# Performance work log

Measured on AMD Instinct MI355X. Metric: run time of the kernel, lower is better.

## Reference

```python
import jax, jax.numpy as jnp
import numpy as np

# Production-scale dims (see shape_source)
N = 100_000      # total nodes (tokens)
E = 1_600_000    # edges
B = 2_000        # graphs / documents
VOCAB = 50_000
NW = 256         # word_vec width == GraphConv out channels (args.nw)
ENC = 512        # args.enc_nh
K = 100          # args.num_topic
EPS = 1e-5       # BatchNorm eps


def setup_inputs() -> dict:
    key = jax.random.key(0)
    ks = jax.random.split(key, 24)
    idx_x = jax.random.randint(ks[0], (N,), 0, VOCAB)
    idx_w = jnp.ones((1,), jnp.float32)          # scalar self-loop weight
    x_batch = jnp.sort(jax.random.randint(ks[1], (N,), 0, B))
    edge_index = jax.random.randint(ks[2], (2, E), 0, N)
    edge_weight = jax.random.uniform(ks[3], (E,), jnp.float32)
    # Parameters
    s = 0.02
    word_vec = jax.random.normal(ks[4], (VOCAB, NW), jnp.float32) * s
    Wrel = jax.random.normal(ks[5], (NW, NW), jnp.float32) * s   # GraphConv lin_rel
    brel = jnp.zeros((NW,), jnp.float32)
    Wroot = jax.random.normal(ks[6], (NW, NW), jnp.float32) * s  # GraphConv lin_root (no bias)
    bn_gamma = jnp.ones((NW,), jnp.float32)
    bn_beta = jnp.zeros((NW,), jnp.float32)
    W1 = jax.random.normal(ks[7], (ENC, 2 * NW), jnp.float32) * s  # enc2_fc1
    b1 = jnp.zeros((ENC,), jnp.float32)
    W2 = jax.random.normal(ks[8], (ENC, 2 * NW), jnp.float32) * s  # enc2_fc2
    b2 = jnp.zeros((ENC,), jnp.float32)
    Wm = jax.random.normal(ks[9], (K, ENC), jnp.float32) * s       # mean_fc
    bm = jnp.zeros((K,), jnp.float32)
    Wv = jnp.zeros((K, ENC), jnp.float32)                          # logvar_fc zero-init
    bv = jnp.zeros((K,), jnp.float32)
    Wphi = jax.random.normal(ks[10], (K, 2 * NW + ENC), jnp.float32) * s  # phi_fc
    bphi = jnp.zeros((K,), jnp.float32)
    return dict(idx_x=idx_x, idx_w=idx_w, x_batch=x_batch, edge_index=edge_index,
                edge_weight=edge_weight, word_vec=word_vec, Wrel=Wrel, brel=brel,
                Wroot=Wroot, bn_gamma=bn_gamma, bn_beta=bn_beta, W1=W1, b1=b1,
                W2=W2, b2=b2, Wm=Wm, bm=bm, Wv=Wv, bv=bv, Wphi=Wphi, bphi=bphi)


def reference(idx_x, idx_w, x_batch, edge_index, edge_weight, word_vec,
              Wrel, brel, Wroot, bn_gamma, bn_beta, W1, b1, W2, b2,
              Wm, bm, Wv, bv, Wphi, bphi):
    # Embedding gather
    x = word_vec[idx_x]                                # [N, NW]
    src, dst = edge_index[0], edge_index[1]
    # GraphConv with explicit self-loops of weight idx_w (diag edges in original)
    msg = edge_weight[:, None] * x[src]                # [E, NW]
    aggr = jax.ops.segment_sum(msg, dst, num_segments=N) + idx_w * x
    h = aggr @ Wrel.T + brel + x @ Wroot.T             # lin_rel(aggr) + lin_root(x)
    # BatchNorm1d (training-mode batch stats, biased variance) + tanh
    mu = jnp.mean(h, axis=0)
    var = jnp.mean((h - mu) ** 2, axis=0)
    enc1 = jnp.tanh((h - mu) * jax.lax.rsqrt(var + EPS) * bn_gamma + bn_beta)
    enc1 = jnp.concatenate([enc1, x], axis=-1)         # [N, 2*NW]
    # GLU gate
    enc2 = jax.nn.sigmoid(enc1 @ W1.T + b1) * jnp.tanh(enc1 @ W2.T + b2)  # [N, ENC]
    # Scatter-sum pooling per document (dropout is identity in eval)
    pooled = jax.ops.segment_sum(enc2, x_batch, num_segments=B)            # [B, ENC]
    mean = pooled @ Wm.T + bm                          # [B, K]
    logvar = pooled @ Wv.T + bv                        # [B, K]
    # Gather re-expansion + softmax
    word_embed = jnp.concatenate([enc1, pooled[x_batch]], axis=-1)         # [N, 2*NW+ENC]
    phi = jax.nn.softmax(word_embed @ Wphi.T + bphi, axis=-1)              # [N, K]
    return mean, logvar, phi
```

## Files before the change

### kernel.cpp

```cpp
#include <hip/hip_runtime.h>
#include <hip/hip_bf16.h>

#define NW 256
#define D2 512
#define PK 1024
#define BM 128
#define BK 64
#define DPB 8
#define SCHUNK 1024

typedef unsigned short u16;
typedef short bf16x8 __attribute__((ext_vector_type(8)));
typedef float f32x4 __attribute__((ext_vector_type(4)));

__device__ __forceinline__ float bf2f(u16 u) {
    union { unsigned u; float f; } v; v.u = ((unsigned)u) << 16; return v.f;
}
__device__ __forceinline__ u16 f2bf(float f) {
    union { float f; unsigned u; } v; v.f = f;
    unsigned u = v.u;
    return (u16)((u + 0x7fffu + ((u >> 16) & 1u)) >> 16);
}
__device__ __forceinline__ float tanh_fast(float x) {
    return 1.f - 2.f / (1.f + __expf(2.f * x));
}

__device__ __forceinline__ void stage_tile(const u16* __restrict__ base, int row0, int maxrow,
                                           int ldk, int k0, u16* lds, int tid) {
    int w = tid >> 6, l = tid & 63;
#pragma unroll
    for (int i = 0; i < 4; ++i) {
        int loadIdx = i * 256 + w * 64 + l;
        int row = loadIdx >> 3, s = loadIdx & 7;
        int srow = row0 + row; if (srow > maxrow) srow = maxrow;
        int scol = k0 + ((s ^ (row & 7)) << 3);
        const u16* g = base + (size_t)srow * ldk + scol;
        u16* ld = lds + (size_t)(i * 256 + w * 64) * 8;
        __builtin_amdgcn_global_load_lds((const __attribute__((address_space(1))) void*)g,
                                         (__attribute__((address_space(3))) void*)ld, 16, 0, 0);
    }
}

__device__ __forceinline__ bf16x8 lds_frag(const u16* lds, int row, int kc, int g) {
    int byte = (row << 7) + (kc << 6) + (g << 4);
    byte ^= (row & 7) << 4;
    return *(const bf16x8*)((const char*)lds + byte);
}

__global__ void k_wprep(const float* __restrict__ Wrel, const float* __restrict__ Wroot,
                        const float* __restrict__ W1, const float* __restrict__ W2,
                        const float* __restrict__ Wphi,
                        u16* __restrict__ wcat, u16* __restrict__ wglu,
                        u16* __restrict__ wphib, float* __restrict__ sums,
                        float* __restrict__ sumsq, int K) {
    int i = blockIdx.x * blockDim.x + threadIdx.x;
    if (i < NW * D2) {
        int c = i >> 9, k = i & 511;
        float v = (k < NW) ? Wrel[c * NW + k] : Wroot[c * NW + (k - NW)];
        wcat[i] = f2bf(v);
    }
    if (i < 1024 * 512) {
        int row = i >> 9, k = i & 511;
        int c = row >> 7, j = row & 127;
        int sub = j >> 5, jj = j & 31;
        int half = sub & 1, colgrp = sub >> 1;
        int col = c * 64 + colgrp * 32 + jj;
        float v = half ? W2[(size_t)col * D2 + k] : W1[(size_t)col * D2 + k];
        wglu[i] = f2bf(v);
    }
    if (i < 128 * 1024) {
        int r = i >> 10, k = i & 1023;
        wphib[i] = f2bf(r < K ? Wphi[(size_t)r * PK + k] : 0.f);
    }
    if (i < NW) { sums[i] = 0.f; sumsq[i] = 0.f; }
}

__global__ void k_gather(const int* __restrict__ idx, const float* __restrict__ wv,
                         u16* __restrict__ X, int N) {
    int row = blockIdx.x * 4 + (threadIdx.x >> 6);
    int lane = threadIdx.x & 63;
    if (row < N) {
        int id = idx[row];
        float4 v = *(const float4*)(wv + (size_t)id * NW + lane * 4);
        ushort4 o;
        o.x = f2bf(v.x); o.y = f2bf(v.y); o.z = f2bf(v.z); o.w = f2bf(v.w);
        *(ushort4*)(X + (size_t)row * D2 + NW + lane * 4) = o;
    }
}

__global__ void k_hist(const int* __restrict__ ei, int* __restrict__ deg, int E) {
    int e = blockIdx.x * blockDim.x + threadIdx.x;
    if (e < E) atomicAdd(&deg[ei[E + e]], 1);
}
__global__ __launch_bounds__(256) void k_scan1(const int* __restrict__ deg,
                                               int* __restrict__ bsum, int N) {
    int b = blockIdx.x, t = threadIdx.x;
    int base = b * SCHUNK;
    int s = 0;
#pragma unroll
    for (int j = 0; j < SCHUNK / 256; ++j) {
        int idx = base + j * 256 + t;
        if (idx < N) s += deg[idx];
    }
    __shared__ int ls[256];
    ls[t] = s; __syncthreads();
    for (int d = 128; d > 0; d >>= 1) {
        if (t < d) ls[t] += ls[t + d];
        __syncthreads();
    }
    if (t == 0) bsum[b] = ls[0];
}
__global__ __launch_bounds__(256) void k_scan2(int* __restrict__ bsum,
                                               int* __restrict__ rowptr, int NB, int N) {
    int t = threadIdx.x;
    int v = (t < NB) ? bsum[t] : 0;
    __shared__ int ls[256];
    ls[t] = v; __syncthreads();
    for (int d = 1; d < 256; d <<= 1) {
        int x = (t >= d) ? ls[t - d] : 0;
        __syncthreads();
        ls[t] += x;
        __syncthreads();
    }
    if (t < NB) bsum[t] = ls[t] - v;
    if (t == 255) rowptr[N] = ls[255];
}
__global__ __launch_bounds__(256) void k_scan3(int* __restrict__ deg,
                                               const int* __restrict__ bsum,
                                               int* __restrict__ rowptr, int N) {
    int b = blockIdx.x, t = threadIdx.x;
    int tbase = b * SCHUNK + t * 4;
    int loc[4];
    int s = 0;
#pragma unroll
    for (int j = 0; j < 4; ++j) {
        int idx = tbase + j;
        loc[j] = (idx < N) ? deg[idx] : 0;
        s += loc[j];
    }
    __shared__ int ls[256];
    ls[t] = s; __syncthreads();
    for (int d = 1; d < 256; d <<= 1) {
        int x = (t >= d) ? ls[t - d] : 0;
        __syncthreads();
        ls[t] += x;
        __syncthreads();
    }
    int run = bsum[b] + ls[t] - s;
#pragma unroll
    for (int j = 0; j < 4; ++j) {
        int idx = tbase + j;
        if (idx < N) { rowptr[idx] = run; run += loc[j]; deg[idx] = 0; }
    }
}
__global__ void k_scatter(const int* __restrict__ ei, const float* __restrict__ ew,
                          const int* __restrict__ rowptr, int* __restrict__ cursor,
                          int* __restrict__ ecols, float* __restrict__ evals, int E) {
    int e = blockIdx.x * blockDim.x + threadIdx.x;
    if (e < E) {
        int d = ei[E + e];
        int p = rowptr[d] + atomicAdd(&cursor[d], 1);
        ecols[p] = ei[e];
        evals[p] = ew[e];
    }
}

__global__ void k_spmm(const int* __restrict__ rowptr, const int* __restrict__ ecols,
                       const float* __restrict__ evals, const float* __restrict__ idxw,
                       u16* __restrict__ X, int N) {
    int n = blockIdx.x * 4 + (threadIdx.x >> 6);
    int l = threadIdx.x & 63;
    if (n >= N) return;
    int half = l >> 5, li = l & 31;
    float a[8];
    bf16x8 xv = *(const bf16x8*)(X + (size_t)n * D2 + NW + li * 8);
    float iw = idxw[0];
#pragma unroll
    for (int j = 0; j < 8; ++j) a[j] = half ? 0.f : iw * bf2f((u16)xv[j]);
    int r0 = rowptr[n], r1 = rowptr[n + 1];
#pragma unroll 4
    for (int e = r0 + half; e < r1; e += 2) {
        int s = ecols[e];
        float w = evals[e];
        bf16x8 v = *(const bf16x8*)(X + (size_t)s * D2 + NW + li * 8);
#pragma unroll
        for (int j = 0; j < 8; ++j) a[j] += w * bf2f((u16)v[j]);
    }
#pragma unroll
    for (int j = 0; j < 8; ++j) a[j] += __shfl_xor(a[j], 32);
    if (half == 0) {
        bf16x8 o;
#pragma unroll
        for (int j = 0; j < 8; ++j) o[j] = (short)f2bf(a[j]);
        *(bf16x8*)(X + (size_t)n * D2 + li * 8) = o;
    }
}

__global__ __launch_bounds__(256) void k_gemm_h(const u16* __restrict__ A, const u16* __restrict__ W,
                                                const float* __restrict__ brel, u16* __restrict__ H,
                                                float* __restrict__ sums, float* __restrict__ sumsq,
                                                int M, int MT) {
    int b = blockIdx.x;
    int xcd = b & 7, j = b >> 3;
    int chunk = j & 1;
    int panel = (j >> 1) * 8 + xcd;
    if (panel >= MT) return;
    __shared__ u16 As[2][BM * BK], Ws[2][BM * BK];
    int tid = threadIdx.x;
    int w = tid >> 6, l = tid & 63, l16 = l & 15, g = l >> 4;
    int wr = w >> 1, wc = w & 1;
    int row0 = panel * BM;
    const u16* wbase = W + (size_t)chunk * 128 * D2;
    f32x4 acc[4][4];
#pragma unroll
    for (int m = 0; m < 4; ++m)
#pragma unroll
        for (int n = 0; n < 4; ++n) { f32x4 z = {0.f, 0.f, 0.f, 0.f}; acc[m][n] = z; }

    stage_tile(A, row0, M - 1, D2, 0, As[0], tid);
    stage_tile(wbase, 0, 127, D2, 0, Ws[0], tid);
    __syncthreads();
    int buf = 0;
    for (int kt = 0; kt < 8; ++kt) {
        if (kt < 7) {
            stage_tile(A, row0, M - 1, D2, (kt + 1) * BK, As[buf ^ 1], tid);
            stage_tile(wbase, 0, 127, D2, (kt + 1) * BK, Ws[buf ^ 1], tid);
        }
#pragma unroll
        for (int kc = 0; kc < 2; ++kc) {
            bf16x8 af[4], bfr[4];
#pragma unroll
            for (int m = 0; m < 4; ++m) af[m] = lds_frag(As[buf], wr * 64 + m * 16 + l16, kc, g);
#pragma unroll
            for (int n = 0; n < 4; ++n) bfr[n] = lds_frag(Ws[buf], wc * 64 + n * 16 + l16, kc, g);
#pragma unroll
            for (int n = 0; n < 4; ++n)
#pragma unroll
                for (int m = 0; m < 4; ++m)
                    acc[m][n] = __builtin_amdgcn_mfma_f32_16x16x32_bf16(af[m], bfr[n], acc[m][n], 0, 0, 0);
        }
        __syncthreads();
        buf ^= 1;
    }
    float* ssum = (float*)As[0];
    float* ssq  = ssum + 128;
    if (tid < 128) { ssum[tid] = 0.f; ssq[tid] = 0.f; }
    __syncthreads();
    int colb = chunk * 128;
#pragma unroll
    for (int n = 0; n < 4; ++n) {
        int lcol = wc * 64 + n * 16 + l16;
        int col = colb + lcol;
        float bb = brel[col];
        float cs = 0.f, cq = 0.f;
#pragma unroll
        for (int m = 0; m < 4; ++m) {
            int row = row0 + wr * 64 + m * 16 + g * 4;
#pragma unroll
            for (int r = 0; r < 4; ++r) {
                if (row + r < M) {
                    float v = acc[m][n][r] + bb;
                    H[(size_t)(row + r) * NW + col] = f2bf(v);
                    cs += v; cq += v * v;
                }
            }
        }
        cs += __shfl_xor(cs, 16); cs += __shfl_xor(cs, 32);
        cq += __shfl_xor(cq, 16); cq += __shfl_xor(cq, 32);
        if (g == 0) { atomicAdd(&ssum[lcol], cs); atomicAdd(&ssq[lcol], cq); }
    }
    __syncthreads();
    if (tid < 128) {
        atomicAdd(&sums[colb + tid], ssum[tid]);
        atomicAdd(&sumsq[colb + tid], ssq[tid]);
    }
}

__global__ void k_bnprep(const float* __restrict__ sums, const float* __restrict__ sumsq,
                         const float* __restrict__ gamma, const float* __restrict__ beta,
                         float* __restrict__ bnab, int N) {
    int c = threadIdx.x;
    float inv = 1.f / (float)N;
    float mu = sums[c] * inv;
    float var = sumsq[c] * inv - mu * mu;
    float rs = rsqrtf(var + 1e-5f);
    float a = rs * gamma[c];
    bnab[c] = a;
    bnab[NW + c] = beta[c] - mu * a;
}

__global__ void k_enc1(const u16* __restrict__ H, const float* __restrict__ bnab,
                       u16* __restrict__ X, int N) {
    int row = blockIdx.x * 4 + (threadIdx.x >> 6);
    int lane = threadIdx.x & 63;
    if (row >= N) return;
    int c = lane * 4;
    ushort4 hv = *(const ushort4*)(H + (size_t)row * NW + c);
    ushort4 o;
    o.x = f2bf(tanh_fast(bf2f(hv.x) * bnab[c + 0] + bnab[NW + c + 0]));
    o.y = f2bf(tanh_fast(bf2f(hv.y) * bnab[c + 1] + bnab[NW + c + 1]));
    o.z = f2bf(tanh_fast(bf2f(hv.z) * bnab[c + 2] + bnab[NW + c + 2]));
    o.w = f2bf(tanh_fast(bf2f(hv.w) * bnab[c + 3] + bnab[NW + c + 3]));
    *(ushort4*)(X + (size_t)row * D2 + c) = o;
}

__global__ __launch_bounds__(256) void k_glu(const u16* __restrict__ A, const u16* __restrict__ Wp,
                                             const float* __restrict__ b1, const float* __restrict__ b2,
                                             u16* __restrict__ enc2, int M, int MT) {
    int b = blockIdx.x;
    int xcd = b & 7, j = b >> 3;
    int chunk = j & 7;
    int panel = (j >> 3) * 8 + xcd;
    if (panel >= MT) return;
    __shared__ u16 As[2][BM * BK], Ws[2][BM * BK];
    int tid = threadIdx.x;
    int w = tid >> 6, l = tid & 63, l16 = l & 15, g = l >> 4;
    int wr = w >> 1, wc = w & 1;
    int row0 = panel * BM;
    const u16* wbase = Wp + (size_t)chunk * 128 * D2;
    f32x4 acc[4][4];
#pragma unroll
    for (int m = 0; m < 4; ++m)
#pragma unroll
        for (int n = 0; n < 4; ++n) { f32x4 z = {0.f, 0.f, 0.f, 0.f}; acc[m][n] = z; }

    stage_tile(A, row0, M - 1, D2, 0, As[0], tid);
    stage_tile(wbase, 0, 127, D2, 0, Ws[0], tid);
    __syncthreads();
    int buf = 0;
    for (int kt = 0; kt < 8; ++kt) {
        if (kt < 7) {
            stage_tile(A, row0, M - 1, D2, (kt + 1) * BK, As[buf ^ 1], tid);
            stage_tile(wbase, 0, 127, D2, (kt + 1) * BK, Ws[buf ^ 1], tid);
        }
#pragma unroll
        for (int kc = 0; kc < 2; ++kc) {
            bf16x8 af[4], bfr[4];
#pragma unroll
            for (int m = 0; m < 4; ++m) af[m] = lds_frag(As[buf], wr * 64 + m * 16 + l16, kc, g);
#pragma unroll
            for (int n = 0; n < 4; ++n) bfr[n] = lds_frag(Ws[buf], wc * 64 + n * 16 + l16, kc, g);
#pragma unroll
            for (int n = 0; n < 4; ++n)
#pragma unroll
                for (int m = 0; m < 4; ++m)
                    acc[m][n] = __builtin_amdgcn_mfma_f32_16x16x32_bf16(af[m], bfr[n], acc[m][n], 0, 0, 0);
        }
        __syncthreads();
        buf ^= 1;
    }
    int colb = chunk * 64 + wc * 32;
#pragma unroll
    for (int n = 0; n < 2; ++n) {
        int col = colb + n * 16 + l16;
        float f1 = b1[col], f2 = b2[col];
#pragma unroll
        for (int m = 0; m < 4; ++m) {
            int row = row0 + wr * 64 + m * 16 + g * 4;
#pragma unroll
            for (int r = 0; r < 4; ++r) {
                if (row + r < M) {
                    float g1 = acc[m][n][r] + f1;
                    float g2 = acc[m][n + 2][r] + f2;
                    float sg = 1.f / (1.f + __expf(-g1));
                    enc2[(size_t)(row + r) * D2 + col] = f2bf(sg * tanh_fast(g2));
                }
            }
        }
    }
}

__global__ void k_docptr(const int* __restrict__ xb, int* __restrict__ dp, int N, int B) {
    int b = blockIdx.x * blockDim.x + threadIdx.x;
    if (b <= B) {
        int lo = 0, hi = N;
        while (lo < hi) { int mid = (lo + hi) >> 1; if (xb[mid] < b) lo = mid + 1; else hi = mid; }
        dp[b] = lo;
    }
}

__global__ void k_pool(const u16* __restrict__ enc2, const int* __restrict__ dp,
                       float* __restrict__ pooled, u16* __restrict__ pooledb, int B) {
    int b = blockIdx.x, t = threadIdx.x;
    int r0 = dp[b], r1 = dp[b + 1];
    float a0 = 0.f, a1 = 0.f;
    for (int r = r0; r < r1; ++r) {
        a0 += bf2f(enc2[(size_t)r * D2 + t]);
        a1 += bf2f(enc2[(size_t)r * D2 + 256 + t]);
    }
    pooled[(size_t)b * D2 + t] = a0;
    pooled[(size_t)b * D2 + 256 + t] = a1;
    pooledb[(size_t)b * D2 + t] = f2bf(a0);
    pooledb[(size_t)b * D2 + 256 + t] = f2bf(a1);
}

__global__ __launch_bounds__(128) void k_meanvar(const float* __restrict__ pooled,
                                                 const float* __restrict__ Wm,
                                                 const float* __restrict__ bm,
                                                 const float* __restrict__ Wv,
                                                 const float* __restrict__ bv,
                                                 float* __restrict__ out, int B, int K) {
    __shared__ float sp[DPB][D2];
    int b0 = blockIdx.x * DPB;
    int t = threadIdx.x;
    for (int i = t; i < DPB * D2; i += 128) {
        int d = i >> 9, c = i & 511;
        int b = b0 + d;
        sp[d][c] = (b < B) ? pooled[(size_t)b * D2 + c] : 0.f;
    }
    __syncthreads();
    if (t < K) {
        float m[DPB], v[DPB];
#pragma unroll
        for (int d = 0; d < DPB; ++d) { m[d] = 0.f; v[d] = 0.f; }
        const float* wm = Wm + (size_t)t * D2;
        const float* wv = Wv + (size_t)t * D2;
        for (int c = 0; c < D2; ++c) {
            float a = wm[c], bb = wv[c];
#pragma unroll
            for (int d = 0; d < DPB; ++d) {
                m[d] += sp[d][c] * a;
                v[d] += sp[d][c] * bb;
            }
        }
        float mb = bm[t], vb = bv[t];
#pragma unroll
        for (int d = 0; d < DPB; ++d) {
            int b = b0 + d;
            if (b < B) {
                out[(size_t)b * K + t] = m[d] + mb;
                out[(size_t)B * K + (size_t)b * K + t] = v[d] + vb;
            }
        }
    }
}

__device__ __forceinline__ void stage_phiA(const u16* __restrict__ X, const u16* __restrict__ PB,
                                           const int* __restrict__ xb, int row0, int M,
                                           int k0, u16* lds, int tid) {
    int w = tid >> 6, l = tid & 63;
#pragma unroll
    for (int i = 0; i < 4; ++i) {
        int loadIdx = i * 256 + w * 64 + l;
        int row = loadIdx >> 3, s = loadIdx & 7;
        int srow = row0 + row; if (srow >= M) srow = M - 1;
        int scol = k0 + ((s ^ (row & 7)) << 3);
        const u16* gsrc = (scol < D2) ? X + (size_t)srow * D2 + scol
                                      : PB + (size_t)xb[srow] * D2 + (scol - D2);
        u16* ld = lds + (size_t)(i * 256 + w * 64) * 8;
        __builtin_amdgcn_global_load_lds((const __attribute__((address_space(1))) void*)gsrc,
                                         (__attribute__((address_space(3))) void*)ld, 16, 0, 0);
    }
}

__global__ __launch_bounds__(256) void k_phi(const u16* __restrict__ X, const u16* __restrict__ PB,
                                             const int* __restrict__ xb, const u16* __restrict__ Wp,
                                             const float* __restrict__ bphi, float* __restrict__ out,
                                             int M, int B, int K) {
    __shared__ u16 As[2][BM * BK], Ws[2][BM * BK];
    int tid = threadIdx.x;
    int w = tid >> 6, l = tid & 63, l16 = l & 15, g = l >> 4;
    int row0 = blockIdx.x * BM;
    f32x4 acc[2][8];
#pragma unroll
    for (int m = 0; m < 2; ++m)
#pragma unroll
        for (int n = 0; n < 8; ++n) { f32x4 z = {0.f, 0.f, 0.f, 0.f}; acc[m][n] = z; }

    stage_phiA(X, PB, xb, row0, M, 0, As[0], tid);
    stage_tile(Wp, 0, 127, PK, 0, Ws[0], tid);
    __syncthreads();
    int buf = 0;
    for (int kt = 0; kt < 16; ++kt) {
        if (kt < 15) {
            stage_phiA(X, PB, xb, row0, M, (kt + 1) * BK, As[buf ^ 1], tid);
            stage_tile(Wp, 0, 127, PK, (kt + 1) * BK, Ws[buf ^ 1], tid);
        }
#pragma unroll
        for (int kc = 0; kc < 2; ++kc) {
            bf16x8 a0 = lds_frag(As[buf], w * 32 + l16, kc, g);
            bf16x8 a1 = lds_frag(As[buf], w * 32 + 16 + l16, kc, g);
#pragma unroll
            for (int n = 0; n < 8; ++n) {
                bf16x8 bb = lds_frag(Ws[buf], n * 16 + l16, kc, g);
                acc[0][n] = __builtin_amdgcn_mfma_f32_16x16x32_bf16(a0, bb, acc[0][n], 0, 0, 0);
                acc[1][n] = __builtin_amdgcn_mfma_f32_16x16x32_bf16(a1, bb, acc[1][n], 0, 0, 0);
            }
        }
        __syncthreads();
        buf ^= 1;
    }
    size_t outoff = (size_t)2 * B * K;
#pragma unroll
    for (int m = 0; m < 2; ++m) {
        int rb = row0 + w * 32 + m * 16 + g * 4;
#pragma unroll
        for (int r = 0; r < 4; ++r) {
            int row = rb + r;
            if (row >= M) continue;
            float v[7];
            float mx = -1e30f;
#pragma unroll
            for (int n = 0; n < 7; ++n) {
                int col = n * 16 + l16;
                float t = (col < K) ? acc[m][n][r] + bphi[col] : -1e30f;
                v[n] = t;
                mx = fmaxf(mx, t);
            }
            mx = fmaxf(mx, __shfl_xor(mx, 1));
            mx = fmaxf(mx, __shfl_xor(mx, 2));
            mx = fmaxf(mx, __shfl_xor(mx, 4));
            mx = fmaxf(mx, __shfl_xor(mx, 8));
            float s = 0.f;
#pragma unroll
            for (int n = 0; n < 7; ++n) {
                int col = n * 16 + l16;
                float e = (col < K) ? __expf(v[n] - mx) : 0.f;
                v[n] = e;
                s += e;
            }
            s += __shfl_xor(s, 1);
            s += __shfl_xor(s, 2);
            s += __shfl_xor(s, 4);
            s += __shfl_xor(s, 8);
            float inv = 1.f / s;
#pragma unroll
            for (int n = 0; n < 7; ++n) {
                int col = n * 16 + l16;
                if (col < K) out[outoff + (size_t)row * K + col] = v[n] * inv;
            }
        }
    }
}

extern "C" void kernel_launch(void* const* d_in, const int* in_sizes, int n_in,
                              void* d_out, int out_size, void* d_ws, size_t ws_size,
                              hipStream_t stream) {
    const int N = in_sizes[0];
    const int E = in_sizes[4];
    const int K = in_sizes[16];
    const int B = (int)(((size_t)out_size - (size_t)N * K) / (2 * (size_t)K));

    const int*   idx_x   = (const int*)d_in[0];
    const float* idx_w   = (const float*)d_in[1];
    const int*   x_batch = (const int*)d_in[2];
    const int*   ei      = (const int*)d_in[3];
    const float* ew      = (const float*)d_in[4];
    const float* word_vec= (const float*)d_in[5];
    const float* Wrel    = (const float*)d_in[6];
    const float* brel    = (const float*)d_in[7];
    const float* Wroot   = (const float*)d_in[8];
    const float* gamma   = (const float*)d_in[9];
    const float* beta    = (const float*)d_in[10];
    const float* W1      = (const float*)d_in[11];
    const float* b1      = (const float*)d_in[12];
    const float* W2      = (const float*)d_in[13];
    const float* b2      = (const float*)d_in[14];
    const float* Wm      = (const float*)d_in[15];
    const float* bm      = (const float*)d_in[16];
    const float* Wv      = (const float*)d_in[17];
    const float* bv      = (const float*)d_in[18];
    const float* Wphi    = (const float*)d_in[19];
    const float* bphi    = (const float*)d_in[20];
    float* out = (float*)d_out;

    char* p = (char*)d_ws;
    auto take = [&](size_t bytes) -> char* {
        char* r = p;
        p += (bytes + 255) & ~(size_t)255;
        return r;
    };
    u16* X = (u16*)take((size_t)N * D2 * 2);
    char* Ybase = take((size_t)N * D2 * 2);
    u16*   hb   = (u16*)Ybase;
    u16*   enc2 = (u16*)Ybase;
    char* q = Ybase;
    auto takeY = [&](size_t bytes) -> char* {
        char* r = q;
        q += (bytes + 255) & ~(size_t)255;
        return r;
    };
    int*   rowptr = (int*)takeY((size_t)(N + 1) * 4);
    int*   cursor = (int*)takeY((size_t)N * 4);
    int*   ecols  = (int*)takeY((size_t)E * 4);
    float* evals  = (float*)takeY((size_t)E * 4);
    u16*   wcat    = (u16*)take((size_t)NW * D2 * 2);
    u16*   wglu    = (u16*)take((size_t)1024 * D2 * 2);
    u16*   wphib   = (u16*)take((size_t)128 * PK * 2);
    int*   docptr  = (int*)take((size_t)(B + 1) * 4);
    float* pooled  = (float*)take((size_t)B * D2 * 4);
    u16*   pooledb = (u16*)take((size_t)B * D2 * 2);
    float* sums    = (float*)take(NW * 4);
    float* sumsq   = (float*)take(NW * 4);
    float* bnab    = (float*)take(2 * NW * 4);
    int*   bsum    = (int*)take(256 * 4);

    if ((size_t)(p - (char*)d_ws) > ws_size) return;

    hipMemsetAsync(cursor, 0, (size_t)N * 4, stream);

    k_wprep<<<(1024 * 512 + 255) / 256, 256, 0, stream>>>(Wrel, Wroot, W1, W2, Wphi,
                                                          wcat, wglu, wphib, sums, sumsq, K);

    k_gather<<<(N + 3) / 4, 256, 0, stream>>>(idx_x, word_vec, X, N);
    k_hist<<<(E + 255) / 256, 256, 0, stream>>>(ei, cursor, E);
    int NB = (N + SCHUNK - 1) / SCHUNK;
    k_scan1<<<NB, 256, 0, stream>>>(cursor, bsum, N);
    k_scan2<<<1, 256, 0, stream>>>(bsum, rowptr, NB, N);
    k_scan3<<<NB, 256, 0, stream>>>(cursor, bsum, rowptr, N);
    k_scatter<<<(E + 255) / 256, 256, 0, stream>>>(ei, ew, rowptr, cursor, ecols, evals, E);
    k_spmm<<<(N + 3) / 4, 256, 0, stream>>>(rowptr, ecols, evals, idx_w, X, N);

    int MT = (N + BM - 1) / BM;
    int P8 = (MT + 7) / 8;
    k_gemm_h<<<P8 * 8 * 2, 256, 0, stream>>>(X, wcat, brel, hb, sums, sumsq, N, MT);
    k_bnprep<<<1, NW, 0, stream>>>(sums, sumsq, gamma, beta, bnab, N);
    k_enc1<<<(N + 3) / 4, 256, 0, stream>>>(hb, bnab, X, N);

    k_glu<<<P8 * 8 * 8, 256, 0, stream>>>(X, wglu, b1, b2, enc2, N, MT);

    k_docptr<<<(B + 1 + 255) / 256, 256, 0, stream>>>(x_batch, docptr, N, B);
    k_pool<<<B, 256, 0, stream>>>(enc2, docptr, pooled, pooledb, B);
    k_meanvar<<<(B + DPB - 1) / DPB, 128, 0, stream>>>(pooled, Wm, bm, Wv, bv, out, B, K);
    k_phi<<<MT, 256, 0, stream>>>(X, pooledb, x_batch, wphib, bphi, out, N, B, K);
}
```

Before: 769.8 us.

## Loop all weight chunks inside one block per row panel in GEMM kernels

k_gemm_h and k_glu now launch one block per 128-row panel, and each block loops over every output column chunk itself, keeping the staging pipeline running across chunk boundaries. The epilogue runs inside the loop when a chunk finishes, and the accumulators are then reset. This removes the XCD-swizzled multi-block grid and the shared-memory partial reduction of BN statistics, which now go straight to global atomics. The A panel is still re-fetched for each chunk (through L2), the grid shrinks to about 782 blocks, which cuts parallelism on 256 CUs, and global atomic traffic for the BN sums goes up.

```diff
diff --git a/kernel.cpp b/kernel.cpp
--- a/kernel.cpp
+++ b/kernel.cpp
@@ -199,18 +199,13 @@
 __global__ __launch_bounds__(256) void k_gemm_h(const u16* __restrict__ A, const u16* __restrict__ W,
                                                 const float* __restrict__ brel, u16* __restrict__ H,
                                                 float* __restrict__ sums, float* __restrict__ sumsq,
-                                                int M, int MT) {
-    int b = blockIdx.x;
-    int xcd = b & 7, j = b >> 3;
-    int chunk = j & 1;
-    int panel = (j >> 1) * 8 + xcd;
-    if (panel >= MT) return;
+                                                int M) {
+    int panel = blockIdx.x;
     __shared__ u16 As[2][BM * BK], Ws[2][BM * BK];
     int tid = threadIdx.x;
     int w = tid >> 6, l = tid & 63, l16 = l & 15, g = l >> 4;
     int wr = w >> 1, wc = w & 1;
     int row0 = panel * BM;
-    const u16* wbase = W + (size_t)chunk * 128 * D2;
     f32x4 acc[4][4];
 #pragma unroll
     for (int m = 0; m < 4; ++m)
@@ -218,13 +213,15 @@
         for (int n = 0; n < 4; ++n) { f32x4 z = {0.f, 0.f, 0.f, 0.f}; acc[m][n] = z; }
 
     stage_tile(A, row0, M - 1, D2, 0, As[0], tid);
-    stage_tile(wbase, 0, 127, D2, 0, Ws[0], tid);
+    stage_tile(W, 0, 127, D2, 0, Ws[0], tid);
     __syncthreads();
     int buf = 0;
-    for (int kt = 0; kt < 8; ++kt) {
-        if (kt < 7) {
-            stage_tile(A, row0, M - 1, D2, (kt + 1) * BK, As[buf ^ 1], tid);
-            stage_tile(wbase, 0, 127, D2, (kt + 1) * BK, Ws[buf ^ 1], tid);
+    for (int it = 0; it < 16; ++it) {
+        int chunk = it >> 3, kt = it & 7;
+        if (it < 15) {
+            int nxt = it + 1, nchunk = nxt >> 3, nkt = nxt & 7;
+            stage_tile(A, row0, M - 1, D2, nkt * BK, As[buf ^ 1], tid);
+            stage_tile(W + (size_t)nchunk * 128 * D2, 0, 127, D2, nkt * BK, Ws[buf ^ 1], tid);
         }
 #pragma unroll
         for (int kc = 0; kc < 2; ++kc) {
@@ -239,40 +236,36 @@
                 for (int m = 0; m < 4; ++m)
                     acc[m][n] = __builtin_amdgcn_mfma_f32_16x16x32_bf16(af[m], bfr[n], acc[m][n], 0, 0, 0);
         }
+        if (kt == 7) {
+            int colb = chunk * 128;
+#pragma unroll
+            for (int n = 0; n < 4; ++n) {
+                int col = colb + wc * 64 + n * 16 + l16;
+                float bb = brel[col];
+                float cs = 0.f, cq = 0.f;
+#pragma unroll
+                for (int m = 0; m < 4; ++m) {
+                    int row = row0 + wr * 64 + m * 16 + g * 4;
+#pragma unroll
+                    for (int r = 0; r < 4; ++r) {
+                        if (row + r < M) {
+                            float v = acc[m][n][r] + bb;
+                            H[(size_t)(row + r) * NW + col] = f2bf(v);
+                            cs += v; cq += v * v;
+                        }
+                    }
+                }
+                cs += __shfl_xor(cs, 16); cs += __shfl_xor(cs, 32);
+                cq += __shfl_xor(cq, 16); cq += __shfl_xor(cq, 32);
+                if (g == 0) { atomicAdd(&sums[col], cs); atomicAdd(&sumsq[col], cq); }
+            }
+#pragma unroll
+            for (int m = 0; m < 4; ++m)
+#pragma unroll
+                for (int n = 0; n < 4; ++n) { f32x4 z = {0.f, 0.f, 0.f, 0.f}; acc[m][n] = z; }
+        }
         __syncthreads();
         buf ^= 1;
-    }
-    float* ssum = (float*)As[0];
-    float* ssq  = ssum + 128;
-    if (tid < 128) { ssum[tid] = 0.f; ssq[tid] = 0.f; }
-    __syncthreads();
-    int colb = chunk * 128;
-#pragma unroll
-    for (int n = 0; n < 4; ++n) {
-        int lcol = wc * 64 + n * 16 + l16;
-        int col = colb + lcol;
-        float bb = brel[col];
-        float cs = 0.f, cq = 0.f;
-#pragma unroll
-        for (int m = 0; m < 4; ++m) {
-            int row = row0 + wr * 64 + m * 16 + g * 4;
-#pragma unroll
-            for (int r = 0; r < 4; ++r) {
-                if (row + r < M) {
-                    float v = acc[m][n][r] + bb;
-                    H[(size_t)(row + r) * NW + col] = f2bf(v);
-                    cs += v; cq += v * v;
-                }
-            }
-        }
-        cs += __shfl_xor(cs, 16); cs += __shfl_xor(cs, 32);
-        cq += __shfl_xor(cq, 16); cq += __shfl_xor(cq, 32);
-        if (g == 0) { atomicAdd(&ssum[lcol], cs); atomicAdd(&ssq[lcol], cq); }
-    }
-    __syncthreads();
-    if (tid < 128) {
-        atomicAdd(&sums[colb + tid], ssum[tid]);
-        atomicAdd(&sumsq[colb + tid], ssq[tid]);
     }
 }
 
@@ -306,18 +299,13 @@
 
 __global__ __launch_bounds__(256) void k_glu(const u16* __restrict__ A, const u16* __restrict__ Wp,
                                              const float* __restrict__ b1, const float* __restrict__ b2,
-                                             u16* __restrict__ enc2, int M, int MT) {
-    int b = blockIdx.x;
-    int xcd = b & 7, j = b >> 3;
-    int chunk = j & 7;
-    int panel = (j >> 3) * 8 + xcd;
-    if (panel >= MT) return;
+                                             u16* __restrict__ enc2, int M) {
+    int panel = blockIdx.x;
     __shared__ u16 As[2][BM * BK], Ws[2][BM * BK];
     int tid = threadIdx.x;
     int w = tid >> 6, l = tid & 63, l16 = l & 15, g = l >> 4;
     int wr = w >> 1, wc = w & 1;
     int row0 = panel * BM;
-    const u16* wbase = Wp + (size_t)chunk * 128 * D2;
     f32x4 acc[4][4];
 #pragma unroll
     for (int m = 0; m < 4; ++m)
@@ -325,13 +313,15 @@
         for (int n = 0; n < 4; ++n) { f32x4 z = {0.f, 0.f, 0.f, 0.f}; acc[m][n] = z; }
 
     stage_tile(A, row0, M - 1, D2, 0, As[0], tid);
-    stage_tile(wbase, 0, 127, D2, 0, Ws[0], tid);
+    stage_tile(Wp, 0, 127, D2, 0, Ws[0], tid);
     __syncthreads();
     int buf = 0;
-    for (int kt = 0; kt < 8; ++kt) {
-        if (kt < 7) {
-            stage_tile(A, row0, M - 1, D2, (kt + 1) * BK, As[buf ^ 1], tid);
-            stage_tile(wbase, 0, 127, D2, (kt + 1) * BK, Ws[buf ^ 1], tid);
+    for (int it = 0; it < 64; ++it) {
+        int chunk = it >> 3, kt = it & 7;
+        if (it < 63) {
+            int nxt = it + 1, nchunk = nxt >> 3, nkt = nxt & 7;
+            stage_tile(A, row0, M - 1, D2, nkt * BK, As[buf ^ 1], tid);
+            stage_tile(Wp + (size_t)nchunk * 128 * D2, 0, 127, D2, nkt * BK, Ws[buf ^ 1], tid);
         }
 #pragma unroll
         for (int kc = 0; kc < 2; ++kc) {
@@ -346,27 +336,33 @@
                 for (int m = 0; m < 4; ++m)
                     acc[m][n] = __builtin_amdgcn_mfma_f32_16x16x32_bf16(af[m], bfr[n], acc[m][n], 0, 0, 0);
         }
+        if (kt == 7) {
+            int colb = chunk * 64 + wc * 32;
+#pragma unroll
+            for (int n = 0; n < 2; ++n) {
+                int col = colb + n * 16 + l16;
+                float f1 = b1[col], f2 = b2[col];
+#pragma unroll
+                for (int m = 0; m < 4; ++m) {
+                    int row = row0 + wr * 64 + m * 16 + g * 4;
+#pragma unroll
+                    for (int r = 0; r < 4; ++r) {
+                        if (row + r < M) {
+                            float g1 = acc[m][n][r] + f1;
+                            float g2 = acc[m][n + 2][r] + f2;
+                            float sg = 1.f / (1.f + __expf(-g1));
+                            enc2[(size_t)(row + r) * D2 + col] = f2bf(sg * tanh_fast(g2));
+                        }
+                    }
+                }
+            }
+#pragma unroll
+            for (int m = 0; m < 4; ++m)
+#pragma unroll
+                for (int n = 0; n < 4; ++n) { f32x4 z = {0.f, 0.f, 0.f, 0.f}; acc[m][n] = z; }
+        }
         __syncthreads();
         buf ^= 1;
-    }
-    int colb = chunk * 64 + wc * 32;
-#pragma unroll
-    for (int n = 0; n < 2; ++n) {
-        int col = colb + n * 16 + l16;
-        float f1 = b1[col], f2 = b2[col];
-#pragma unroll
-        for (int m = 0; m < 4; ++m) {
-            int row = row0 + wr * 64 + m * 16 + g * 4;
-#pragma unroll
-            for (int r = 0; r < 4; ++r) {
-                if (row + r < M) {
-                    float g1 = acc[m][n][r] + f1;
-                    float g2 = acc[m][n + 2][r] + f2;
-                    float sg = 1.f / (1.f + __expf(-g1));
-                    enc2[(size_t)(row + r) * D2 + col] = f2bf(sg * tanh_fast(g2));
-                }
-            }
-        }
     }
 }
 
@@ -612,12 +608,11 @@
     k_spmm<<<(N + 3) / 4, 256, 0, stream>>>(rowptr, ecols, evals, idx_w, X, N);
 
     int MT = (N + BM - 1) / BM;
-    int P8 = (MT + 7) / 8;
-    k_gemm_h<<<P8 * 8 * 2, 256, 0, stream>>>(X, wcat, brel, hb, sums, sumsq, N, MT);
+    k_gemm_h<<<MT, 256, 0, stream>>>(X, wcat, brel, hb, sums, sumsq, N);
     k_bnprep<<<1, NW, 0, stream>>>(sums, sumsq, gamma, beta, bnab, N);
     k_enc1<<<(N + 3) / 4, 256, 0, stream>>>(hb, bnab, X, N);
 
-    k_glu<<<P8 * 8 * 8, 256, 0, stream>>>(X, wglu, b1, b2, enc2, N, MT);
+    k_glu<<<MT, 256, 0, stream>>>(X, wglu, b1, b2, enc2, N);
 
     k_docptr<<<(B + 1 + 255) / 256, 256, 0, stream>>>(x_batch, docptr, N, B);
     k_pool<<<B, 256, 0, stream>>>(enc2, docptr, pooled, pooledb, B);
```

After: 1.198 ms. +55.7%, slower.
